# Kernel tuning notes

Measured on AMD Instinct MI355X. Metric: run time of the kernel, lower is better.

Reference implementation:

```python
import jax, jax.numpy as jnp
import numpy as np

N = 50000      # nodes
E = 800000     # edges (avg degree 16)
D = 128        # in_dim == hidden_dim
CD = 3         # coord_dim (SE(3))
L = 3          # num_layers


def setup_inputs() -> dict:
    key = jax.random.key(0)
    ks = jax.random.split(key, 10)
    s = np.float32(1.0 / np.sqrt(D))
    return {
        "x": jax.random.normal(ks[0], (N, D), jnp.float32),
        "pos": jax.random.normal(ks[1], (N, CD), jnp.float32),
        "edge_index": jax.random.randint(ks[2], (2, E), 0, N, dtype=jnp.int32),
        # per-layer stacked params (in_dim == hidden_dim so all layers stack)
        "Wl": jax.random.normal(ks[3], (L, D, D), jnp.float32) * s,
        "bl": jnp.zeros((L, D), jnp.float32),
        "Wc": jax.random.normal(ks[4], (L, D, 1), jnp.float32) * s,
        "bc": jnp.zeros((L, 1), jnp.float32),
        "WR": jax.random.normal(ks[5], (L, D, CD * CD), jnp.float32) * s,
        "bR": jnp.zeros((L, CD * CD), jnp.float32),
        "Wt": jax.random.normal(ks[6], (L, D, CD), jnp.float32) * s,
        "bt": jnp.zeros((L, CD), jnp.float32),
        # final fc
        "Wf": jax.random.normal(ks[7], (D, D), jnp.float32) * s,
        "bf": jnp.zeros((D,), jnp.float32),
    }


def reference(x, pos, edge_index, Wl, bl, Wc, bc, WR, bR, Wt, bt, Wf, bf):
    src, dst = edge_index[0], edge_index[1]
    n = x.shape[0]
    # R defaults to identity, t to zeros (R_dict/t_dict None path)
    R = jnp.broadcast_to(jnp.eye(CD, dtype=x.dtype), (n, CD, CD))
    t = jnp.zeros_like(pos)
    for i in range(L):
        h = x @ Wl[i] + bl[i]                          # (N, D)  per-edge-type linear
        # MessagePassing aggr='add': message x_j = h[src], scatter-add at dst
        out = jax.ops.segment_sum(h[src], dst, num_segments=n)  # (N, D)
        pos = pos + (out @ Wc[i] + bc[i])              # (N,3) + (N,1) broadcast
        R_upd = (out @ WR[i] + bR[i]).reshape(n, CD, CD)
        Q = jnp.linalg.qr(R_upd)[0]                    # orthonormalize rotation update
        R = Q @ R
        t = t + (out @ Wt[i] + bt[i])
        x = out
    z = x @ Wf + bf
    return z, pos, R, t
```

## Files before the change

### kernel.cpp

```cpp
#include <hip/hip_runtime.h>
#include <hip/hip_fp16.h>

typedef _Float16 half8 __attribute__((ext_vector_type(8)));
typedef float floatx4 __attribute__((ext_vector_type(4)));

#define NHC 16
#define WCOLS (128 + NHC)

__device__ inline void qr3_q(const double A[3][3], double Q[3][3]){
  double a[3][3];
#pragma unroll
  for (int r = 0; r < 3; r++)
#pragma unroll
    for (int c = 0; c < 3; c++) a[r][c] = A[r][c];

  double v1[3] = {1.0, 0.0, 0.0};
  double tau1 = 0.0;
  {
    double xn2 = a[1][0]*a[1][0] + a[2][0]*a[2][0];
    if (xn2 != 0.0){
      double alpha = a[0][0];
      double beta = -copysign(sqrt(alpha*alpha + xn2), alpha);
      tau1 = (beta - alpha) / beta;
      double inv = 1.0 / (alpha - beta);
      v1[1] = a[1][0] * inv;
      v1[2] = a[2][0] * inv;
#pragma unroll
      for (int c = 1; c < 3; c++){
        double w = a[0][c] + v1[1]*a[1][c] + v1[2]*a[2][c];
        double tw = tau1 * w;
        a[0][c] -= tw;
        a[1][c] -= tw * v1[1];
        a[2][c] -= tw * v1[2];
      }
    }
  }
  double tau2 = 0.0, v2 = 0.0;
  {
    double x2 = a[2][1];
    if (x2 != 0.0){
      double alpha = a[1][1];
      double beta = -copysign(sqrt(alpha*alpha + x2*x2), alpha);
      tau2 = (beta - alpha) / beta;
      v2 = x2 / (alpha - beta);
    }
  }
  double M[3][3] = {{1.0, 0.0, 0.0},
                    {0.0, 1.0 - tau2, -tau2*v2},
                    {0.0, -tau2*v2, 1.0 - tau2*v2*v2}};
#pragma unroll
  for (int c = 0; c < 3; c++){
    double w = v1[0]*M[0][c] + v1[1]*M[1][c] + v1[2]*M[2][c];
#pragma unroll
    for (int r = 0; r < 3; r++)
      Q[r][c] = M[r][c] - tau1 * v1[r] * w;
  }
}

__device__ inline void se3_node(int n, const float* __restrict__ dsws,
                                const float* __restrict__ bc, const float* __restrict__ bR,
                                const float* __restrict__ bt, const float* __restrict__ pos_in,
                                float* __restrict__ pos_o, float* __restrict__ R_o,
                                float* __restrict__ t_o, int layer, int N){
  float ds[13];
#pragma unroll
  for (int c = 0; c < 13; c++) ds[c] = dsws[(size_t)c*N + n];

  double A[3][3], Q[3][3];
#pragma unroll
  for (int r = 0; r < 3; r++)
#pragma unroll
    for (int c = 0; c < 3; c++)
      A[r][c] = (double)ds[1 + r*3 + c] + (double)bR[r*3 + c];
  qr3_q(A, Q);

  double pd = (double)ds[0] + (double)bc[0];
#pragma unroll
  for (int c = 0; c < 3; c++){
    double base = (layer == 0) ? (double)pos_in[n*3 + c] : (double)pos_o[n*3 + c];
    pos_o[n*3 + c] = (float)(base + pd);
  }

  if (layer == 0){
#pragma unroll
    for (int r = 0; r < 3; r++)
#pragma unroll
      for (int c = 0; c < 3; c++)
        R_o[n*9 + r*3 + c] = (float)Q[r][c];
  } else {
    double Rold[3][3];
#pragma unroll
    for (int r = 0; r < 3; r++)
#pragma unroll
      for (int c = 0; c < 3; c++)
        Rold[r][c] = (double)R_o[n*9 + r*3 + c];
#pragma unroll
    for (int r = 0; r < 3; r++)
#pragma unroll
      for (int c = 0; c < 3; c++){
        double s = Q[r][0]*Rold[0][c] + Q[r][1]*Rold[1][c] + Q[r][2]*Rold[2][c];
        R_o[n*9 + r*3 + c] = (float)s;
      }
  }
#pragma unroll
  for (int c = 0; c < 3; c++){
    double base = (layer == 0) ? 0.0 : (double)t_o[n*3 + c];
    t_o[n*3 + c] = (float)(base + (double)ds[10 + c] + (double)bt[c]);
  }
}

__global__ void k_prep_w(const float* __restrict__ Wl, const float* __restrict__ Wf,
                         const float* __restrict__ Wc, const float* __restrict__ WR,
                         const float* __restrict__ Wt, _Float16* __restrict__ wTx){
  int t = blockIdx.x*256 + threadIdx.x;
  if (t >= 4*WCOLS*128) return;
  int l = t / (WCOLS*128);
  int rem = t - l*(WCOLS*128);
  int n = rem >> 7;
  int k = rem & 127;
  float v = 0.f;
  if (n < 128){
    const float* W = (l < 3) ? (Wl + (size_t)l*16384) : Wf;
    v = W[k*128 + n];
  } else if (l > 0){
    int h = n - 128, hl = l - 1;
    if (h == 0)       v = Wc[(size_t)hl*128 + k];
    else if (h < 10)  v = WR[(size_t)hl*128*9 + k*9 + (h-1)];
    else if (h < 13)  v = Wt[(size_t)hl*128*3 + k*3 + (h-10)];
  }
  wTx[t] = (_Float16)v;
}

__launch_bounds__(256)
__global__ void k_bin(const int* __restrict__ src, const int* __restrict__ dst,
                      int E, int nbuck, int capB,
                      int* __restrict__ cursor, int* __restrict__ binned){
  __shared__ int cnt[128];
  __shared__ int segbase[128];
  const int tid = threadIdx.x;
  for (int t = tid; t < nbuck; t += 256) cnt[t] = 0;
  __syncthreads();
  const int e0 = blockIdx.x*4096 + tid;
  int pk[16], bk[16];
#pragma unroll
  for (int j = 0; j < 16; j++){
    int e = e0 + j*256;
    if (e < E){
      int d = dst[e], s = src[e];
      bk[j] = d >> 9;
      pk[j] = (s << 9) | (d & 511);
      atomicAdd(&cnt[bk[j]], 1);
    } else bk[j] = -1;
  }
  __syncthreads();
  for (int t = tid; t < nbuck; t += 256){
    int c = cnt[t];
    if (c > 0) segbase[t] = t*capB + atomicAdd(&cursor[t], c);
    cnt[t] = 0;
  }
  __syncthreads();
#pragma unroll
  for (int j = 0; j < 16; j++){
    if (bk[j] >= 0){
      int ord = atomicAdd(&cnt[bk[j]], 1);
      binned[segbase[bk[j]] + ord] = pk[j];
    }
  }
}

__launch_bounds__(256)
__global__ void k_build(const int* __restrict__ binned, const int* __restrict__ cursor,
                        int N, int capB, int capC,
                        int2* __restrict__ sd, int* __restrict__ csr){
  __shared__ int deg[512];
  __shared__ int lstart[512];
  __shared__ int cnt2[512];
  __shared__ int scn[256];
  const int b = blockIdx.x, tid = threadIdx.x;
  deg[tid] = 0; deg[tid+256] = 0;
  __syncthreads();
  const int nE = cursor[b];
  const int gbase = b*capB;
  for (int i = tid; i < nE; i += 256)
    atomicAdd(&deg[binned[gbase + i] & 511], 1);
  __syncthreads();
  const int d0 = deg[2*tid], d1 = deg[2*tid+1];
  const int p0 = (d0+7)&~7,  p1 = (d1+7)&~7;
  scn[tid] = p0 + p1;
  __syncthreads();
#pragma unroll
  for (int off = 1; off < 256; off <<= 1){
    int add = (tid >= off) ? scn[tid-off] : 0;
    __syncthreads();
    scn[tid] += add;
    __syncthreads();
  }
  const int ex = scn[tid] - (p0 + p1);
  const int csrb = b*capC;
  lstart[2*tid]   = ex;
  lstart[2*tid+1] = ex + p0;
  cnt2[2*tid] = 0; cnt2[2*tid+1] = 0;
  const int n0 = b*512 + 2*tid, n1 = n0 + 1;
  if (n0 < N) sd[n0] = make_int2(csrb + ex, p0);
  if (n1 < N) sd[n1] = make_int2(csrb + ex + p0, p1);
  __syncthreads();
  for (int i = tid; i < nE; i += 256){
    int v = binned[gbase + i];
    int dl = v & 511, s = v >> 9;
    int ord = atomicAdd(&cnt2[dl], 1);
    csr[csrb + lstart[dl] + ord] = s;
  }
  for (int j = d0; j < p0; j++) csr[csrb + lstart[2*tid]   + j] = N;
  for (int j = d1; j < p1; j++) csr[csrb + lstart[2*tid+1] + j] = N;
}

__launch_bounds__(256)
__global__ void k_gemm_mfma(const void* __restrict__ Xin, const _Float16* __restrict__ Wt,
                            const float* __restrict__ bias, void* __restrict__ Hout,
                            float* __restrict__ dsws,
                            int M, int in_fp32, int out_fp32, int zero_pad){
  const int wave = threadIdx.x >> 6;
  const int lane = threadIdx.x & 63;
  const int quad = lane >> 4;
  const int l16  = lane & 15;
  const int rbase = blockIdx.x*64 + (wave & 1)*32;
  const int cthi = wave >> 1;
  const int ctb = cthi*4;

  const _Float16* X16 = (const _Float16*)Xin;
  const float*    X32 = (const float*)Xin;

  floatx4 acc[2][5] = {};
#pragma unroll
  for (int kc = 0; kc < 4; kc++){
    half8 af[2];
#pragma unroll
    for (int rt = 0; rt < 2; rt++){
      int r = rbase + rt*16 + l16;
      r = (r < M) ? r : (M - 1);
      if (in_fp32){
        const float* p = X32 + (size_t)r*128 + kc*32 + quad*8;
        float4 f0 = *(const float4*)p;
        float4 f1 = *(const float4*)(p + 4);
        half8 a;
        a[0]=(_Float16)f0.x; a[1]=(_Float16)f0.y; a[2]=(_Float16)f0.z; a[3]=(_Float16)f0.w;
        a[4]=(_Float16)f1.x; a[5]=(_Float16)f1.y; a[6]=(_Float16)f1.z; a[7]=(_Float16)f1.w;
        af[rt] = a;
      } else {
        af[rt] = *(const half8*)(X16 + (size_t)r*128 + kc*32 + quad*8);
      }
    }
#pragma unroll
    for (int ct = 0; ct < 5; ct++){
      if (ct == 4 && cthi == 0) continue;
      half8 bf = *(const half8*)(Wt + (size_t)((ctb+ct)*16 + l16)*128 + kc*32 + quad*8);
      acc[0][ct] = __builtin_amdgcn_mfma_f32_16x16x32_f16(af[0], bf, acc[0][ct], 0, 0, 0);
      acc[1][ct] = __builtin_amdgcn_mfma_f32_16x16x32_f16(af[1], bf, acc[1][ct], 0, 0, 0);
    }
  }
#pragma unroll
  for (int rt = 0; rt < 2; rt++){
#pragma unroll
    for (int ct = 0; ct < 5; ct++){
      if (ct == 4 && cthi == 0) continue;
      int col = (ctb+ct)*16 + l16;
      float bv = (col < 128) ? bias[col] : 0.f;
#pragma unroll
      for (int reg = 0; reg < 4; reg++){
        int r = rbase + rt*16 + quad*4 + reg;
        if (r < M){
          float v = acc[rt][ct][reg] + bv;
          if (col < 128){
            if (out_fp32) ((float*)Hout)[(size_t)r*128 + col] = v;
            else          ((_Float16*)Hout)[(size_t)r*128 + col] = (_Float16)v;
          } else if (col < 141){
            dsws[(size_t)(col-128)*M + r] = v;
          }
        } else if (zero_pad && r == M && !out_fp32 && col < 128){
          ((_Float16*)Hout)[(size_t)r*128 + col] = (_Float16)0.f;
        }
      }
    }
  }
}

__launch_bounds__(256)
__global__ void k_agg(const _Float16* __restrict__ H, const int* __restrict__ csr,
                      const int2* __restrict__ sd, _Float16* __restrict__ Xout,
                      int N, int agg_blocks,
                      const float* __restrict__ dsws, const float* __restrict__ bc,
                      const float* __restrict__ bR, const float* __restrict__ bt,
                      const float* __restrict__ pos_in, float* __restrict__ pos_o,
                      float* __restrict__ R_o, float* __restrict__ t_o, int se3_layer){
  if ((int)blockIdx.x >= agg_blocks){
    int n = (blockIdx.x - agg_blocks)*256 + threadIdx.x;
    if (n < N) se3_node(n, dsws, bc, bR, bt, pos_in, pos_o, R_o, t_o, se3_layer, N);
    return;
  }
  const int wave = threadIdx.x >> 6;
  const int lane = threadIdx.x & 63;
  const int node = blockIdx.x*4 + wave;
  if (node >= N) return;
  int2 s = sd[node];
  const int s0 = s.x, degp = s.y;
  const unsigned int* Hu = (const unsigned int*)H;
  float acc0 = 0.f, acc1 = 0.f;
  for (int base = 0; base < degp; base += 64){
    int myidx = csr[s0 + base + lane];
    int m = degp - base; m = (m < 64) ? m : 64;
    for (int k = 0; k < m; k += 8){
      unsigned int v[8];
#pragma unroll
      for (int j = 0; j < 8; j++){
        int idx = __builtin_amdgcn_readlane(myidx, k + j);
        v[j] = Hu[(size_t)idx*64 + lane];
      }
#pragma unroll
      for (int j = 0; j < 8; j++){
        float2 f = __half22float2(*(__half2*)&v[j]);
        acc0 += f.x; acc1 += f.y;
      }
    }
  }
  __half2 ho = __floats2half2_rn(acc0, acc1);
  ((unsigned int*)Xout)[(size_t)node*64 + lane] = *(unsigned int*)&ho;
}

__launch_bounds__(256)
__global__ void k_se3(const float* __restrict__ dsws,
                      const float* __restrict__ bc, const float* __restrict__ bR,
                      const float* __restrict__ bt, const float* __restrict__ pos_in,
                      float* __restrict__ pos_o, float* __restrict__ R_o, float* __restrict__ t_o,
                      int layer, int N){
  int n = blockIdx.x*256 + threadIdx.x;
  if (n < N) se3_node(n, dsws, bc, bR, bt, pos_in, pos_o, R_o, t_o, layer, N);
}

extern "C" void kernel_launch(void* const* d_in, const int* in_sizes, int n_in,
                              void* d_out, int out_size, void* d_ws, size_t ws_size,
                              hipStream_t stream){
  const float* x0  = (const float*)d_in[0];
  const float* pos = (const float*)d_in[1];
  const int*   ei  = (const int*)d_in[2];
  const float* Wl  = (const float*)d_in[3];
  const float* bl  = (const float*)d_in[4];
  const float* Wc  = (const float*)d_in[5];
  const float* bc  = (const float*)d_in[6];
  const float* WR  = (const float*)d_in[7];
  const float* bR  = (const float*)d_in[8];
  const float* Wt  = (const float*)d_in[9];
  const float* bt  = (const float*)d_in[10];
  const float* Wf  = (const float*)d_in[11];
  const float* bf  = (const float*)d_in[12];

  const int N = in_sizes[0] / 128;
  const int E = in_sizes[2] / 2;
  const int* srcp = ei;
  const int* dstp = ei + E;

  float* z_out = (float*)d_out;
  float* pos_o = z_out + (size_t)N*128;
  float* R_o   = pos_o + (size_t)N*3;
  float* t_o   = R_o   + (size_t)N*9;

  const int nbuck = (N + 511) >> 9;
  const int capB  = (((E + nbuck - 1)/nbuck)*5/4 + 256 + 63) & ~63;
  const int capC  = capB + 512*7;

  char* ws = (char*)d_ws;
  size_t off = 0;
  auto alloc = [&](size_t bytes)->char*{
    char* p = ws + off; off += (bytes + 511) & ~(size_t)511; return p;
  };
  _Float16* buf0h = (_Float16*)alloc((size_t)N*128*2);
  _Float16* buf1h = (_Float16*)alloc((size_t)(N+1)*128*2);
  _Float16* wTx   = (_Float16*)alloc((size_t)4*WCOLS*128*2);
  float* dsws   = (float*)alloc((size_t)13*N*4);
  int2*  sd     = (int2*) alloc((size_t)N*8);
  int*   cursor = (int*)  alloc((size_t)nbuck*4);
  int*   binned = (int*)  alloc((size_t)nbuck*capB*4);
  int*   csr    = (int*)  alloc((size_t)nbuck*capC*4);

  hipMemsetAsync(cursor, 0, (size_t)nbuck*4, stream);

  k_prep_w<<<dim3((4*WCOLS*128 + 255)/256), dim3(256), 0, stream>>>(Wl, Wf, Wc, WR, Wt, wTx);
  k_bin   <<<dim3((E + 4095)/4096), dim3(256), 0, stream>>>(srcp, dstp, E, nbuck, capB, cursor, binned);
  k_build <<<dim3(nbuck), dim3(256), 0, stream>>>(binned, cursor, N, capB, capC, sd, csr);

  const int gemm_blocks_pad = (N + 64)/64;
  const int gemm_blocks     = (N + 63)/64;
  const int agg_blocks      = (N + 3)/4;
  const int se3_blocks      = (N + 255)/256;

  const void* xcur = (const void*)x0;
  for (int layer = 0; layer < 3; layer++){
    k_gemm_mfma<<<dim3(gemm_blocks_pad), dim3(256), 0, stream>>>(
        xcur, wTx + (size_t)layer*WCOLS*128, bl + (size_t)layer*128, (void*)buf1h,
        dsws, N, (layer == 0) ? 1 : 0, 0, 1);
    int extra = (layer >= 1) ? se3_blocks : 0;
    k_agg<<<dim3(agg_blocks + extra), dim3(256), 0, stream>>>(
        buf1h, csr, sd, buf0h, N, agg_blocks,
        dsws, bc + (layer-1), bR + (size_t)(layer-1)*9, bt + (size_t)(layer-1)*3,
        pos, pos_o, R_o, t_o, layer - 1);
    xcur = (const void*)buf0h;
  }
  k_gemm_mfma<<<dim3(gemm_blocks), dim3(256), 0, stream>>>(
      xcur, wTx + (size_t)3*WCOLS*128, bf, (void*)z_out, dsws, N, 0, 1, 0);
  k_se3<<<dim3(se3_blocks), dim3(256), 0, stream>>>(
      dsws, bc + 2, bR + 18, bt + 6, pos, pos_o, R_o, t_o, 2, N);
}
```

Before: 323.5 us.

## Sort CSR neighbors by source range, hoist A loads, fold cursor reset into prep

CSR construction now orders each node's neighbor list into 8 coarse source-index bands (src >> 13) using per-node sub-bucket counters in shared memory. The goal is to make the aggregation gathers of h[src] more cache-local. The GEMM now loads all four K-chunks of A fragments before running the MFMA loop, so load latency can overlap with compute. The cursor memset is removed and the reset is done inside k_prep_w instead, saving one launch. The cost is 8x larger shared arrays in k_build, which lowers its occupancy, and more registers held in the GEMM.

```diff
diff --git a/kernel.cpp b/kernel.cpp
--- a/kernel.cpp
+++ b/kernel.cpp
@@ -6,6 +6,7 @@
 
 #define NHC 16
 #define WCOLS (128 + NHC)
+#define OSH 13
 
 __device__ inline void qr3_q(const double A[3][3], double Q[3][3]){
   double a[3][3];
@@ -111,8 +112,10 @@
 
 __global__ void k_prep_w(const float* __restrict__ Wl, const float* __restrict__ Wf,
                          const float* __restrict__ Wc, const float* __restrict__ WR,
-                         const float* __restrict__ Wt, _Float16* __restrict__ wTx){
+                         const float* __restrict__ Wt, _Float16* __restrict__ wTx,
+                         int* __restrict__ cursor, int nbuck){
   int t = blockIdx.x*256 + threadIdx.x;
+  if (blockIdx.x == 0 && threadIdx.x < nbuck) cursor[threadIdx.x] = 0;
   if (t >= 4*WCOLS*128) return;
   int l = t / (WCOLS*128);
   int rem = t - l*(WCOLS*128);
@@ -172,20 +175,26 @@
 __global__ void k_build(const int* __restrict__ binned, const int* __restrict__ cursor,
                         int N, int capB, int capC,
                         int2* __restrict__ sd, int* __restrict__ csr){
-  __shared__ int deg[512];
-  __shared__ int lstart[512];
-  __shared__ int cnt2[512];
+  __shared__ int deg2[512*8];
+  __shared__ int lst2[512*8];
+  __shared__ int cnt2[512*8];
   __shared__ int scn[256];
   const int b = blockIdx.x, tid = threadIdx.x;
-  deg[tid] = 0; deg[tid+256] = 0;
+  for (int t = tid; t < 512*8; t += 256){ deg2[t] = 0; cnt2[t] = 0; }
   __syncthreads();
   const int nE = cursor[b];
   const int gbase = b*capB;
-  for (int i = tid; i < nE; i += 256)
-    atomicAdd(&deg[binned[gbase + i] & 511], 1);
-  __syncthreads();
-  const int d0 = deg[2*tid], d1 = deg[2*tid+1];
-  const int p0 = (d0+7)&~7,  p1 = (d1+7)&~7;
+  for (int i = tid; i < nE; i += 256){
+    int v = binned[gbase + i];
+    int o = v >> (9 + OSH);
+    if (o > 7) o = 7;
+    atomicAdd(&deg2[((v & 511) << 3) + o], 1);
+  }
+  __syncthreads();
+  int d0 = 0, d1 = 0;
+#pragma unroll
+  for (int o = 0; o < 8; o++){ d0 += deg2[((2*tid) << 3) + o]; d1 += deg2[((2*tid+1) << 3) + o]; }
+  const int p0 = (d0+7)&~7, p1 = (d1+7)&~7;
   scn[tid] = p0 + p1;
   __syncthreads();
 #pragma unroll
@@ -197,9 +206,14 @@
   }
   const int ex = scn[tid] - (p0 + p1);
   const int csrb = b*capC;
-  lstart[2*tid]   = ex;
-  lstart[2*tid+1] = ex + p0;
-  cnt2[2*tid] = 0; cnt2[2*tid+1] = 0;
+  {
+    int off0 = ex;
+#pragma unroll
+    for (int o = 0; o < 8; o++){ lst2[((2*tid) << 3) + o] = off0; off0 += deg2[((2*tid) << 3) + o]; }
+    int off1 = ex + p0;
+#pragma unroll
+    for (int o = 0; o < 8; o++){ lst2[((2*tid+1) << 3) + o] = off1; off1 += deg2[((2*tid+1) << 3) + o]; }
+  }
   const int n0 = b*512 + 2*tid, n1 = n0 + 1;
   if (n0 < N) sd[n0] = make_int2(csrb + ex, p0);
   if (n1 < N) sd[n1] = make_int2(csrb + ex + p0, p1);
@@ -207,11 +221,12 @@
   for (int i = tid; i < nE; i += 256){
     int v = binned[gbase + i];
     int dl = v & 511, s = v >> 9;
-    int ord = atomicAdd(&cnt2[dl], 1);
-    csr[csrb + lstart[dl] + ord] = s;
-  }
-  for (int j = d0; j < p0; j++) csr[csrb + lstart[2*tid]   + j] = N;
-  for (int j = d1; j < p1; j++) csr[csrb + lstart[2*tid+1] + j] = N;
+    int o = s >> OSH; if (o > 7) o = 7;
+    int ord = atomicAdd(&cnt2[(dl << 3) + o], 1);
+    csr[csrb + lst2[(dl << 3) + o] + ord] = s;
+  }
+  for (int j = d0; j < p0; j++) csr[csrb + ex + j] = N;
+  for (int j = d1; j < p1; j++) csr[csrb + ex + p0 + j] = N;
 }
 
 __launch_bounds__(256)
@@ -230,10 +245,9 @@
   const _Float16* X16 = (const _Float16*)Xin;
   const float*    X32 = (const float*)Xin;
 
-  floatx4 acc[2][5] = {};
+  half8 af[4][2];
 #pragma unroll
   for (int kc = 0; kc < 4; kc++){
-    half8 af[2];
 #pragma unroll
     for (int rt = 0; rt < 2; rt++){
       int r = rbase + rt*16 + l16;
@@ -245,17 +259,22 @@
         half8 a;
         a[0]=(_Float16)f0.x; a[1]=(_Float16)f0.y; a[2]=(_Float16)f0.z; a[3]=(_Float16)f0.w;
         a[4]=(_Float16)f1.x; a[5]=(_Float16)f1.y; a[6]=(_Float16)f1.z; a[7]=(_Float16)f1.w;
-        af[rt] = a;
+        af[kc][rt] = a;
       } else {
-        af[rt] = *(const half8*)(X16 + (size_t)r*128 + kc*32 + quad*8);
-      }
-    }
+        af[kc][rt] = *(const half8*)(X16 + (size_t)r*128 + kc*32 + quad*8);
+      }
+    }
+  }
+
+  floatx4 acc[2][5] = {};
+#pragma unroll
+  for (int kc = 0; kc < 4; kc++){
 #pragma unroll
     for (int ct = 0; ct < 5; ct++){
       if (ct == 4 && cthi == 0) continue;
       half8 bf = *(const half8*)(Wt + (size_t)((ctb+ct)*16 + l16)*128 + kc*32 + quad*8);
-      acc[0][ct] = __builtin_amdgcn_mfma_f32_16x16x32_f16(af[0], bf, acc[0][ct], 0, 0, 0);
-      acc[1][ct] = __builtin_amdgcn_mfma_f32_16x16x32_f16(af[1], bf, acc[1][ct], 0, 0, 0);
+      acc[0][ct] = __builtin_amdgcn_mfma_f32_16x16x32_f16(af[kc][0], bf, acc[0][ct], 0, 0, 0);
+      acc[1][ct] = __builtin_amdgcn_mfma_f32_16x16x32_f16(af[kc][1], bf, acc[1][ct], 0, 0, 0);
     }
   }
 #pragma unroll
@@ -381,9 +400,8 @@
   int*   binned = (int*)  alloc((size_t)nbuck*capB*4);
   int*   csr    = (int*)  alloc((size_t)nbuck*capC*4);
 
-  hipMemsetAsync(cursor, 0, (size_t)nbuck*4, stream);
-
-  k_prep_w<<<dim3((4*WCOLS*128 + 255)/256), dim3(256), 0, stream>>>(Wl, Wf, Wc, WR, Wt, wTx);
+  k_prep_w<<<dim3((4*WCOLS*128 + 255)/256), dim3(256), 0, stream>>>(
+      Wl, Wf, Wc, WR, Wt, wTx, cursor, nbuck);
   k_bin   <<<dim3((E + 4095)/4096), dim3(256), 0, stream>>>(srcp, dstp, E, nbuck, capB, cursor, binned);
   k_build <<<dim3(nbuck), dim3(256), 0, stream>>>(binned, cursor, N, capB, capC, sd, csr);
 
```

Result: no change. 318.7 us (-1.5%).
